# Kernel tuning notes

Hardware: AMD Instinct MI355X
Metric: run time of the kernel (lower is better)

The kernel has to match this reference:

```python
import jax, jax.numpy as jnp
import numpy as np


def setup_inputs() -> dict:
    key = jax.random.key(0)
    k1, k2 = jax.random.split(key)
    N, D = 131072, 128
    features = jax.random.normal(k1, (N, D), dtype=jnp.float32)
    attention_scores = jax.random.normal(k2, (N,), dtype=jnp.float32)
    return {"features": features, "attention_scores": attention_scores, "k": 256}


def _fps(features, attention_scores, k):
    # L2-normalize rows (matches F.normalize(p=2, dim=1) with eps clamp)
    norms = jnp.linalg.norm(features, axis=1, keepdims=True)
    fn = features / jnp.maximum(norms, 1e-12)  # [N, D]

    neg_inf = jnp.float32(-jnp.inf)
    first_idx = jnp.argmax(attention_scores).astype(jnp.int32)
    # Euclidean distance from every point to the first selected point
    d0 = jnp.linalg.norm(fn - fn[first_idx][None, :], axis=1)  # [N]
    min_d = d0.at[first_idx].set(neg_inf)

    def step(min_d, _):
        far = jnp.argmax(min_d).astype(jnp.int32)
        new_d = jnp.linalg.norm(fn - fn[far][None, :], axis=1)
        min_d = jnp.minimum(min_d, new_d).at[far].set(neg_inf)
        return min_d, far

    _, rest = jax.lax.scan(step, min_d, None, length=k - 1)
    return jnp.concatenate([first_idx[None], rest])  # [k] int32


def reference(features, attention_scores, k):
    N = features.shape[0]
    if k >= N:  # k is a static Python int
        return jnp.arange(N, dtype=jnp.int32)
    return _fps(features, attention_scores, k)
```

## Files before the change

kernel.cpp:

```cpp
#include <hip/hip_runtime.h>
#include <math.h>

#define NTHR 1024
#define DD   128
#define SELP 80

typedef unsigned long long ull;

#define FOR8(M) M(0) M(1) M(2) M(3) M(4) M(5) M(6) M(7)

__device__ __forceinline__ ull pkkey(float f, unsigned idx) {
  unsigned u = __float_as_uint(f);
  u = (u & 0x80000000u) ? ~u : (u | 0x80000000u);
  return ((ull)u << 32) | (ull)(~idx);
}

__device__ __forceinline__ ull wredmax(ull v) {
#pragma unroll
  for (int m = 32; m; m >>= 1) {
    ull o = __shfl_xor(v, m, 64);
    v = (o > v) ? o : v;
  }
  return v;
}

__device__ __forceinline__ int roundSyncC(float val, unsigned pidx, int t,
                                          ull* __restrict__ partials,
                                          ull* __restrict__ bcast, int nblk,
                                          ull* s_w, int* s_far,
                                          int tid, int lane, int wid, int blockId) {
  ull key = wredmax(pkkey(val, pidx));
  if (lane == 0) s_w[wid] = key;
  __syncthreads();
  const unsigned tag = (unsigned)(t + 1);
  if (tid == 0) {
    ull m = s_w[0];
#pragma unroll
    for (int i = 1; i < NTHR / 64; ++i) { ull o = s_w[i]; if (o > m) m = o; }
    unsigned idx = ~(unsigned)m;
    ull slotv = (m & 0xFFFFFFFF00000000ull) | ((ull)tag << 17) | (ull)idx;
    __hip_atomic_store(&partials[(t & 1) * nblk + blockId], slotv,
                       __ATOMIC_RELAXED, __HIP_MEMORY_SCOPE_AGENT);
  }
  if (blockId == 0) {
    ull ck = 0;
    if (tid < nblk) {
      ull* slot = &partials[(t & 1) * nblk + tid];
      ull v;
      do {
        v = __hip_atomic_load(slot, __ATOMIC_RELAXED, __HIP_MEMORY_SCOPE_AGENT);
      } while (((unsigned)(v >> 17) & 0x7FFFu) != tag);
      ck = (v & 0xFFFFFFFF00000000ull) | (ull)(~((unsigned)v & 0x1FFFFu));
    }
    ck = wredmax(ck);
    __syncthreads();
    if (lane == 0) s_w[wid] = ck;
    __syncthreads();
    if (tid == 0) {
      ull m = s_w[0];
#pragma unroll
      for (int i = 1; i < NTHR / 64; ++i) { ull o = s_w[i]; if (o > m) m = o; }
      unsigned widx = ~(unsigned)m;
      __hip_atomic_store(&bcast[t & 1], ((ull)tag << 17) | (ull)widx,
                         __ATOMIC_RELAXED, __HIP_MEMORY_SCOPE_AGENT);
      *s_far = (int)widx;
    }
    __syncthreads();
  } else {
    if (tid == 0) {
      ull v;
      do {
        v = __hip_atomic_load(&bcast[t & 1], __ATOMIC_RELAXED, __HIP_MEMORY_SCOPE_AGENT);
      } while (((unsigned)(v >> 17) & 0x7FFFu) != tag);
      *s_far = (int)((unsigned)v & 0x1FFFFu);
    }
    __syncthreads();
  }
  return *s_far;
}

__device__ __forceinline__ void stage(const float* __restrict__ feat, int c,
                                      float* s_sel, float* s_nrm, int tid, int lane) {
  const float* __restrict__ row = feat + (size_t)c * DD;
  if (tid < 64) {
    float x1 = row[lane], x2 = row[lane + 64];
    double s = (double)(x1 * x1) + (double)(x2 * x2);
#pragma unroll
    for (int m = 32; m; m >>= 1) s += __shfl_xor(s, m, 64);
    if (lane == 0) *s_nrm = fmaxf(sqrtf((float)s), 1e-12f);
  }
  __syncthreads();
  const float nm = *s_nrm;
  if (tid < DD) s_sel[tid + ((tid >> 6) << 4)] = row[tid] / nm;
  __syncthreads();
}

__global__ __launch_bounds__(NTHR, 4)
void fps_kernel(const float* __restrict__ feat, const float* __restrict__ att,
                const int* __restrict__ kptr, int* __restrict__ out,
                ull* __restrict__ partials, ull* __restrict__ bcast,
                int N, int nblk) {
  __shared__ float4 s_tile[8][NTHR];
  __shared__ ull s_w[NTHR / 64];
  __shared__ alignas(16) float s_sel[144];
  __shared__ float s_nrm;
  __shared__ int s_far;

  const int tid  = threadIdx.x;
  const int lane = tid & 63;
  const int wid  = tid >> 6;
  const int gid  = blockIdx.x * NTHR + tid;
  const int pidx = gid >> 1;
  const int half = tid & 1;
  const int k    = kptr[0];

  if (k >= N) {
    for (int i = gid; i < N; i += nblk * NTHR) out[i] = i;
    return;
  }

  const float4* __restrict__ qb = reinterpret_cast<const float4*>(feat + (size_t)gid * 64);
  float4 v0 = qb[0], v1 = qb[1], v2 = qb[2],  v3 = qb[3],
         v4 = qb[4], v5 = qb[5], v6 = qb[6],  v7 = qb[7];
  float4 q0 = qb[8], q1 = qb[9], q2 = qb[10], q3 = qb[11],
         q4 = qb[12], q5 = qb[13], q6 = qb[14], q7 = qb[15];

  {
    double a0 = 0.0, a1 = 0.0, a2 = 0.0, a3 = 0.0;
#define NACC(i) a0 += (double)(v##i.x * v##i.x) + (double)(q##i.x * q##i.x); \
                a1 += (double)(v##i.y * v##i.y) + (double)(q##i.y * q##i.y); \
                a2 += (double)(v##i.z * v##i.z) + (double)(q##i.z * q##i.z); \
                a3 += (double)(v##i.w * v##i.w) + (double)(q##i.w * q##i.w);
    FOR8(NACC)
#undef NACC
    double s = (a0 + a1) + (a2 + a3);
    s += __shfl_xor(s, 1, 64);
    float nm = fmaxf(sqrtf((float)s), 1e-12f);
#define DIVV(i) v##i.x /= nm; v##i.y /= nm; v##i.z /= nm; v##i.w /= nm; \
                q##i.x /= nm; q##i.y /= nm; q##i.z /= nm; q##i.w /= nm; \
    asm volatile("" : "+v"(q##i.x), "+v"(q##i.y), "+v"(q##i.z), "+v"(q##i.w));
    FOR8(DIVV)
#undef DIVV
  }

#define STASH(i) s_tile[i][tid] = v##i;
  FOR8(STASH)
#undef STASH

  int far = roundSyncC(att[pidx], (unsigned)pidx, 0, partials, bcast, nblk,
                       s_w, &s_far, tid, lane, wid, blockIdx.x);
  if (gid == 0) out[0] = far;

#define DACC_L(i) { float4 a = s_tile[i][tid]; float4 c = sc[i]; \
    float dx = a.x - c.x, dy = a.y - c.y, dz = a.z - c.z, dw = a.w - c.w; \
    b0 += (double)(dx * dx); b1 += (double)(dy * dy); \
    b2 += (double)(dz * dz); b3 += (double)(dw * dw); }
#define DACC_R(i) { float4 c = sc[8 + i]; \
    float dx = q##i.x - c.x, dy = q##i.y - c.y, dz = q##i.z - c.z, dw = q##i.w - c.w; \
    b0 += (double)(dx * dx); b1 += (double)(dy * dy); \
    b2 += (double)(dz * dz); b3 += (double)(dw * dw); }
#define DIST_TO(dvar) do { \
    const float4* sc = reinterpret_cast<const float4*>(s_sel + half * SELP); \
    double b0 = 0.0, b1 = 0.0, b2 = 0.0, b3 = 0.0; \
    FOR8(DACC_L) \
    FOR8(DACC_R) \
    double ss = (b0 + b1) + (b2 + b3); \
    ss += __shfl_xor(ss, 1, 64); \
    dvar = sqrtf((float)ss); \
  } while (0)

  stage(feat, far, s_sel, &s_nrm, tid, lane);
  float mind;
  DIST_TO(mind);
  if (pidx == far) mind = -__builtin_inff();

  for (int t = 1; t < k; ++t) {
    far = roundSyncC(mind, (unsigned)pidx, t, partials, bcast, nblk,
                     s_w, &s_far, tid, lane, wid, blockIdx.x);
    if (gid == 0) out[t] = far;

    stage(feat, far, s_sel, &s_nrm, tid, lane);
    float d;
    DIST_TO(d);
    mind = fminf(mind, d);
    if (pidx == far) mind = -__builtin_inff();
  }
}

extern "C" void kernel_launch(void* const* d_in, const int* in_sizes, int n_in,
                              void* d_out, int out_size, void* d_ws, size_t ws_size,
                              hipStream_t stream) {
  const float* feat = (const float*)d_in[0];
  const float* att  = (const float*)d_in[1];
  const int*   kptr = (const int*)d_in[2];
  int* out = (int*)d_out;

  const int N    = in_sizes[1];
  const int nblk = (2 * N) / NTHR;

  unsigned char* ws = (unsigned char*)d_ws;
  ull* partials = (ull*)ws;
  ull* bcast    = (ull*)(ws + 4096);

  (void)hipMemsetAsync(d_ws, 0, 8192, stream);
  fps_kernel<<<nblk, NTHR, 0, stream>>>(feat, att, kptr, out, partials, bcast, N, nblk);
}
```

Baseline: 1.376 ms.

## Streamline grid-wide argmax sync with padded slots and replicated broadcast lines

The per-round cross-block argmax is restructured. Each block's partial now sits in its own 64-byte slot, block 0 gathers all 256 partials with a single wavefront (four loads per lane) and no extra block barriers, and the winner is written to 8 replicated broadcast lines so the spinning blocks poll different cache lines. The staging of the selected row also drops one barrier by computing the norm and writing the normalized row within one wavefront. This cuts serialized barrier and polling latency on every one of the k rounds, but it assumes nblk is at most 256 and uses a larger workspace.

```diff
diff --git a/kernel.cpp b/kernel.cpp
--- a/kernel.cpp
+++ b/kernel.cpp
@@ -4,6 +4,9 @@
 #define NTHR 1024
 #define DD   128
 #define SELP 80
+#define SLOTS 8
+#define BCS   16
+#define NBC   8
 
 typedef unsigned long long ull;
 
@@ -24,74 +27,77 @@
   return v;
 }
 
-__device__ __forceinline__ int roundSyncC(float val, unsigned pidx, int t,
-                                          ull* __restrict__ partials,
-                                          ull* __restrict__ bcast, int nblk,
-                                          ull* s_w, int* s_far,
-                                          int tid, int lane, int wid, int blockId) {
+__device__ __forceinline__ int roundSync(float val, unsigned pidx, int t,
+                                         ull* __restrict__ partials,
+                                         ull* __restrict__ bcast, int nblk,
+                                         ull* s_w, int* s_far,
+                                         int tid, int lane, int wid, int blockId) {
   ull key = wredmax(pkkey(val, pidx));
   if (lane == 0) s_w[wid] = key;
   __syncthreads();
   const unsigned tag = (unsigned)(t + 1);
-  if (tid == 0) {
-    ull m = s_w[0];
-#pragma unroll
-    for (int i = 1; i < NTHR / 64; ++i) { ull o = s_w[i]; if (o > m) m = o; }
-    unsigned idx = ~(unsigned)m;
-    ull slotv = (m & 0xFFFFFFFF00000000ull) | ((ull)tag << 17) | (ull)idx;
-    __hip_atomic_store(&partials[(t & 1) * nblk + blockId], slotv,
-                       __ATOMIC_RELAXED, __HIP_MEMORY_SCOPE_AGENT);
+  if (tid < 64) {
+    ull m = (lane < NTHR / 64) ? s_w[lane] : 0ull;
+    m = wredmax(m);
+    if (lane == 0) {
+      unsigned idx = ~(unsigned)m;
+      ull slotv = (m & 0xFFFFFFFF00000000ull) | ((ull)tag << 17) | (ull)idx;
+      __hip_atomic_store(&partials[((t & 1) * nblk + blockId) * SLOTS], slotv,
+                         __ATOMIC_RELAXED, __HIP_MEMORY_SCOPE_AGENT);
+    }
   }
   if (blockId == 0) {
-    ull ck = 0;
-    if (tid < nblk) {
-      ull* slot = &partials[(t & 1) * nblk + tid];
+    if (tid < 64) {
+      ull* base = partials + (size_t)(t & 1) * nblk * SLOTS;
+      ull r0 = 0, r1 = 0, r2 = 0, r3 = 0;
+      unsigned got = 0;
+      do {
+        if (!(got & 1u)) { r0 = __hip_atomic_load(&base[(tid)       * SLOTS], __ATOMIC_RELAXED, __HIP_MEMORY_SCOPE_AGENT); if (((unsigned)(r0 >> 17) & 0x7FFFu) == tag) got |= 1u; }
+        if (!(got & 2u)) { r1 = __hip_atomic_load(&base[(tid +  64) * SLOTS], __ATOMIC_RELAXED, __HIP_MEMORY_SCOPE_AGENT); if (((unsigned)(r1 >> 17) & 0x7FFFu) == tag) got |= 2u; }
+        if (!(got & 4u)) { r2 = __hip_atomic_load(&base[(tid + 128) * SLOTS], __ATOMIC_RELAXED, __HIP_MEMORY_SCOPE_AGENT); if (((unsigned)(r2 >> 17) & 0x7FFFu) == tag) got |= 4u; }
+        if (!(got & 8u)) { r3 = __hip_atomic_load(&base[(tid + 192) * SLOTS], __ATOMIC_RELAXED, __HIP_MEMORY_SCOPE_AGENT); if (((unsigned)(r3 >> 17) & 0x7FFFu) == tag) got |= 8u; }
+      } while (got != 0xFu);
+      ull k0 = (r0 & 0xFFFFFFFF00000000ull) | (ull)(~((unsigned)r0 & 0x1FFFFu));
+      ull k1 = (r1 & 0xFFFFFFFF00000000ull) | (ull)(~((unsigned)r1 & 0x1FFFFu));
+      ull k2 = (r2 & 0xFFFFFFFF00000000ull) | (ull)(~((unsigned)r2 & 0x1FFFFu));
+      ull k3 = (r3 & 0xFFFFFFFF00000000ull) | (ull)(~((unsigned)r3 & 0x1FFFFu));
+      ull ck = k0 > k1 ? k0 : k1;
+      ull ck2 = k2 > k3 ? k2 : k3;
+      ck = ck > ck2 ? ck : ck2;
+      ck = wredmax(ck);
+      unsigned widx = ~(unsigned)ck;
+      ull bv = ((ull)tag << 17) | (ull)widx;
+      if (lane < NBC)
+        __hip_atomic_store(&bcast[((t & 1) * NBC + lane) * BCS], bv,
+                           __ATOMIC_RELAXED, __HIP_MEMORY_SCOPE_AGENT);
+      if (lane == 0) *s_far = (int)widx;
+    }
+  } else {
+    if (tid == 0) {
+      ull* line = &bcast[((t & 1) * NBC + (blockId >> 5)) * BCS];
       ull v;
       do {
-        v = __hip_atomic_load(slot, __ATOMIC_RELAXED, __HIP_MEMORY_SCOPE_AGENT);
-      } while (((unsigned)(v >> 17) & 0x7FFFu) != tag);
-      ck = (v & 0xFFFFFFFF00000000ull) | (ull)(~((unsigned)v & 0x1FFFFu));
-    }
-    ck = wredmax(ck);
-    __syncthreads();
-    if (lane == 0) s_w[wid] = ck;
-    __syncthreads();
-    if (tid == 0) {
-      ull m = s_w[0];
-#pragma unroll
-      for (int i = 1; i < NTHR / 64; ++i) { ull o = s_w[i]; if (o > m) m = o; }
-      unsigned widx = ~(unsigned)m;
-      __hip_atomic_store(&bcast[t & 1], ((ull)tag << 17) | (ull)widx,
-                         __ATOMIC_RELAXED, __HIP_MEMORY_SCOPE_AGENT);
-      *s_far = (int)widx;
-    }
-    __syncthreads();
-  } else {
-    if (tid == 0) {
-      ull v;
-      do {
-        v = __hip_atomic_load(&bcast[t & 1], __ATOMIC_RELAXED, __HIP_MEMORY_SCOPE_AGENT);
+        v = __hip_atomic_load(line, __ATOMIC_RELAXED, __HIP_MEMORY_SCOPE_AGENT);
       } while (((unsigned)(v >> 17) & 0x7FFFu) != tag);
       *s_far = (int)((unsigned)v & 0x1FFFFu);
     }
-    __syncthreads();
-  }
+  }
+  __syncthreads();
   return *s_far;
 }
 
 __device__ __forceinline__ void stage(const float* __restrict__ feat, int c,
-                                      float* s_sel, float* s_nrm, int tid, int lane) {
-  const float* __restrict__ row = feat + (size_t)c * DD;
+                                      float* s_sel, int tid, int lane) {
   if (tid < 64) {
+    const float* __restrict__ row = feat + (size_t)c * DD;
     float x1 = row[lane], x2 = row[lane + 64];
     double s = (double)(x1 * x1) + (double)(x2 * x2);
 #pragma unroll
     for (int m = 32; m; m >>= 1) s += __shfl_xor(s, m, 64);
-    if (lane == 0) *s_nrm = fmaxf(sqrtf((float)s), 1e-12f);
-  }
-  __syncthreads();
-  const float nm = *s_nrm;
-  if (tid < DD) s_sel[tid + ((tid >> 6) << 4)] = row[tid] / nm;
+    float nm = fmaxf(sqrtf((float)s), 1e-12f);
+    s_sel[lane] = x1 / nm;
+    s_sel[SELP + lane] = x2 / nm;
+  }
   __syncthreads();
 }
 
@@ -103,7 +109,6 @@
   __shared__ float4 s_tile[8][NTHR];
   __shared__ ull s_w[NTHR / 64];
   __shared__ alignas(16) float s_sel[144];
-  __shared__ float s_nrm;
   __shared__ int s_far;
 
   const int tid  = threadIdx.x;
@@ -147,8 +152,8 @@
   FOR8(STASH)
 #undef STASH
 
-  int far = roundSyncC(att[pidx], (unsigned)pidx, 0, partials, bcast, nblk,
-                       s_w, &s_far, tid, lane, wid, blockIdx.x);
+  int far = roundSync(att[pidx], (unsigned)pidx, 0, partials, bcast, nblk,
+                      s_w, &s_far, tid, lane, wid, blockIdx.x);
   if (gid == 0) out[0] = far;
 
 #define DACC_L(i) { float4 a = s_tile[i][tid]; float4 c = sc[i]; \
@@ -169,17 +174,17 @@
     dvar = sqrtf((float)ss); \
   } while (0)
 
-  stage(feat, far, s_sel, &s_nrm, tid, lane);
+  stage(feat, far, s_sel, tid, lane);
   float mind;
   DIST_TO(mind);
   if (pidx == far) mind = -__builtin_inff();
 
   for (int t = 1; t < k; ++t) {
-    far = roundSyncC(mind, (unsigned)pidx, t, partials, bcast, nblk,
-                     s_w, &s_far, tid, lane, wid, blockIdx.x);
+    far = roundSync(mind, (unsigned)pidx, t, partials, bcast, nblk,
+                    s_w, &s_far, tid, lane, wid, blockIdx.x);
     if (gid == 0) out[t] = far;
 
-    stage(feat, far, s_sel, &s_nrm, tid, lane);
+    stage(feat, far, s_sel, tid, lane);
     float d;
     DIST_TO(d);
     mind = fminf(mind, d);
@@ -200,8 +205,8 @@
 
   unsigned char* ws = (unsigned char*)d_ws;
   ull* partials = (ull*)ws;
-  ull* bcast    = (ull*)(ws + 4096);
-
-  (void)hipMemsetAsync(d_ws, 0, 8192, stream);
+  ull* bcast    = (ull*)(ws + 2 * 256 * 64);
+
+  (void)hipMemsetAsync(d_ws, 0, 2 * 256 * 64 + 2048, stream);
   fps_kernel<<<nblk, NTHR, 0, stream>>>(feat, att, kptr, out, partials, bcast, N, nblk);
 }
```

Result: slower. 1.462 ms (+6.2%).
